# Performance work log

Hardware: AMD Instinct MI355X
Metric: run time of the kernel (lower is better)

Reference implementation:

```python
import jax, jax.numpy as jnp
import numpy as np

B, M, L = 8, 512, 1024          # batch, block_size, attn_lim (max span)
H, K = 512, 8                   # hidden, heads
D = H // K                      # head_dim = 64
RAMP = 32                       # attn_span_len (soft-mask ramp)
SPAN_INIT = 1.0                 # attn_span_init -> full span, skip_len = 0
SCALE = 1.0 / np.sqrt(D)


def _unskew(X):
    # X: [b, M, M+L] -> [b, M, L]  (relative-position unshift via reshape trick)
    b, m, ml = X.shape
    l = ml - m
    X = X.reshape(b, m * ml)
    X = jnp.pad(X, ((0, 0), (0, m)))
    X = X.reshape(b, m, ml + 1)
    return X[:, :, :l]


def _skew(X):
    # X: [b, M, L] -> [b, M, L+M]  (pad value 0)
    b, m, l = X.shape
    X = jnp.pad(X, ((0, 0), (0, 0), (0, m + 1)))
    X = X.reshape(b, -1)[:, : m * (l + m)]
    return X.reshape(b, m, l + m)


def _heads(x):
    # [B, S, H] -> [B*K, S, D]
    b, s, _ = x.shape
    return x.reshape(b, s, K, D).transpose(0, 2, 1, 3).reshape(b * K, s, D)


def setup_inputs() -> dict:
    key0 = jax.random.key(0)
    ks = jax.random.split(key0, 8)
    s = 0.02
    return {
        "query": jax.random.normal(ks[0], (B, M, H), jnp.float32),
        "key": jax.random.normal(ks[1], (B, M + L, H), jnp.float32),
        "value": jax.random.normal(ks[2], (B, M + L, H), jnp.float32),
        "key_pe": jax.random.normal(ks[3], (1, D, L), jnp.float32) * s,
        "Wq": jax.random.normal(ks[4], (H, H), jnp.float32) * s,
        "Wk": jax.random.normal(ks[5], (H, H), jnp.float32) * s,
        "Wv": jax.random.normal(ks[6], (H, H), jnp.float32) * s,
        "Wo": jax.random.normal(ks[7], (H, H), jnp.float32) * s,
        "span_val": jnp.full((K, 1, 1), SPAN_INIT, jnp.float32),
    }


def reference(query, key, value, key_pe, Wq, Wk, Wv, Wo, span_val):
    # QKV projections (nn.Linear, no bias: y = x @ W.T) + head split
    q = _heads(query @ Wq.T)     # [B*K, M, D]
    k = _heads(key @ Wk.T)       # [B*K, M+L, D]
    v = _heads(value @ Wv.T)     # [B*K, M+L, D]

    # content attention + unskew to relative coordinates
    attn_cont = _unskew(jnp.einsum('bmd,bnd->bmn', q, k))    # [B*K, M, L]
    # positional attention (shared across batch/heads via key_pe[1,D,L])
    attn_pos = jnp.einsum('bmd,dl->bml', q, key_pe[0])       # [B*K, M, L]

    attn = jax.nn.softmax((attn_cont + attn_pos) * SCALE, axis=-1)

    # adaptive span soft mask, per head (skip_len = 0)
    template = jnp.linspace(1.0 - L, 0.0, L, dtype=jnp.float32)        # [L]
    mask = jnp.clip((template + span_val * L) / RAMP + 1.0, 0.0, 1.0)  # [K,1,L]
    attn = (attn.reshape(B, K, M, L) * mask[None]).reshape(B * K, M, L)

    # skew back to absolute coords and contract with values
    out = jnp.matmul(_skew(attn), v)                         # [B*K, M, D]
    out = out.reshape(B, K, M, D).transpose(0, 2, 1, 3).reshape(B, M, H)
    return out @ Wo.T
```

## Files before the change

### kernel.cpp

```cpp
#include <hip/hip_runtime.h>
#include <hip/hip_bf16.h>
#include <type_traits>

typedef __hip_bfloat16 bf16;
typedef short bf16x8 __attribute__((ext_vector_type(8)));
typedef float f32x4 __attribute__((ext_vector_type(4)));
typedef short short4_ __attribute__((ext_vector_type(4)));

#define NB 8
#define SM 512
#define SL 1024
#define SH 512
#define NH 8
#define HD 64
#define SN 1536

static __device__ __forceinline__ short bf_bits(float x) {
  union { bf16 b; short s; } u; u.b = __float2bfloat16(x); return u.s;
}
static __device__ __forceinline__ bf16x8 ld8any(const bf16* p) {
  return *reinterpret_cast<const bf16x8*>(p);
}
static __device__ __forceinline__ bf16x8 ld8any(const float* p) {
  float4 a = *reinterpret_cast<const float4*>(p);
  float4 b = *reinterpret_cast<const float4*>(p + 4);
  bf16x8 r;
  r[0] = bf_bits(a.x); r[1] = bf_bits(a.y); r[2] = bf_bits(a.z); r[3] = bf_bits(a.w);
  r[4] = bf_bits(b.x); r[5] = bf_bits(b.y); r[6] = bf_bits(b.z); r[7] = bf_bits(b.w);
  return r;
}
static __device__ __forceinline__ void st1(bf16* p, float v) { *p = __float2bfloat16(v); }
static __device__ __forceinline__ void st1(float* p, float v) { *p = v; }
static __device__ __forceinline__ f32x4 mfma16(bf16x8 a, bf16x8 b, f32x4 c) {
  return __builtin_amdgcn_mfma_f32_16x16x32_bf16(a, b, c, 0, 0, 0);
}


__global__ __launch_bounds__(256) void prep_all(
    const float* __restrict__ key, const float* __restrict__ value,
    const float* __restrict__ query,
    const float* __restrict__ Wq, const float* __restrict__ Wk,
    const float* __restrict__ Wv, const float* __restrict__ Wo,
    const float* __restrict__ pe,
    bf16* __restrict__ kS, bf16* __restrict__ vS, bf16* __restrict__ qS,
    bf16* __restrict__ Wb, bf16* __restrict__ peF) {
  __shared__ __align__(16) bf16 t[16 * 520];
  const int id = blockIdx.x, tid = threadIdx.x;
  if (id < 1920) {
    const float* src; bf16* dst;
    if (id < 768)       { src = key   + (size_t)id * 8192;
                          dst = kS    + (size_t)id * 8192; }
    else if (id < 1536) { src = value + (size_t)(id - 768) * 8192;
                          dst = vS    + (size_t)(id - 768) * 8192; }
    else if (id < 1792) { src = query + (size_t)(id - 1536) * 8192;
                          dst = qS    + (size_t)(id - 1536) * 8192; }
    else {
      const int s = id - 1792;
      const float* ws_[4] = {Wq, Wk, Wv, Wo};
      src = ws_[s >> 5] + (size_t)(s & 31) * 8192;
      dst = Wb + (size_t)(s >> 5) * 262144 + (size_t)(s & 31) * 8192;
    }
#pragma unroll
    for (int j = 0; j < 4; ++j) {
      const int i = j * 2048 + tid * 8;
      const bf16x8 v = ld8any(src + i);
      *reinterpret_cast<bf16x8*>(&t[(i >> 9) * 520 + (i & 511)]) = v;
    }
    __syncthreads();
#pragma unroll
    for (int j = 0; j < 4; ++j) {
      const int a = j * 2048 + tid * 8;
      const int kt5 = a >> 9, rest = a & 511;
      const int q = rest >> 7, rowl = (rest >> 3) & 15;
      *reinterpret_cast<bf16x8*>(dst + a) =
          *reinterpret_cast<const bf16x8*>(&t[rowl * 520 + kt5 * 32 + q * 8]);
    }
  } else {
    const int idx = (id - 1920) * 256 + tid;
    const int l = idx >> 6, d = idx & 63;
    peF[(size_t)((l >> 4) * 2 + (d >> 5)) * 512
        + (size_t)((((d >> 3) & 3) * 16 + (l & 15)) * 8 + (d & 7))]
      = __float2bfloat16(pe[d * SL + l]);
  }
}

#define T2STR 136

#define GL2(AF, BF, KT)                                                      \
  {                                                                          \
    AF[0] = ld8any(xr +         (size_t)(KT) * 512);                         \
    AF[1] = ld8any(xr + 8192  + (size_t)(KT) * 512);                         \
    AF[2] = ld8any(xr + 16384 + (size_t)(KT) * 512);                         \
    AF[3] = ld8any(xr + 24576 + (size_t)(KT) * 512);                         \
    BF[0] = ld8any(wr +         (size_t)(KT) * 512);                         \
    BF[1] = ld8any(wr + 8192  + (size_t)(KT) * 512);                         \
    BF[2] = ld8any(wr + 16384 + (size_t)(KT) * 512);                         \
    BF[3] = ld8any(wr + 24576 + (size_t)(KT) * 512);                         \
  }

#define MF44(AF, BF)                                                         \
  {                                                                          \
    _Pragma("unroll")                                                        \
    for (int mt = 0; mt < 4; ++mt)                                           \
      _Pragma("unroll")                                                      \
      for (int nt = 0; nt < 4; ++nt)                                         \
        acc[mt][nt] = mfma16(AF[mt], BF[nt], acc[mt][nt]);                   \
  }

template <int MODE, typename TY>
static __device__ __forceinline__ void gemm_dev2(const bf16* __restrict__ XF,
                                                 const bf16* __restrict__ WF,
                                                 TY* __restrict__ Y,
                                                 int xblk, int yblk, bf16* tile) {
  const int tid  = threadIdx.x;
  const int lane = tid & 63, w = tid >> 6;
  const int col16 = lane & 15, quad = lane >> 4;
  const int lane8 = lane * 8;
  const int wm = w >> 1, wn = w & 1;
  const int m0 = xblk * 128 + wm * 64;
  const int n0 = yblk * 128 + wn * 64;
  const bf16* xr = XF + (size_t)(m0 >> 4) * 8192 + lane8;
  const bf16* wr = WF + (size_t)(n0 >> 4) * 8192 + lane8;
  f32x4 acc[4][4];
#pragma unroll
  for (int i = 0; i < 4; ++i)
#pragma unroll
    for (int j = 0; j < 4; ++j) acc[i][j] = f32x4{0.f,0.f,0.f,0.f};

  bf16x8 afA[4], bfA[4], afB[4], bfB[4], afC[4], bfC[4];
  GL2(afA, bfA, 0);
  GL2(afB, bfB, 1);
  __builtin_amdgcn_sched_barrier(0);
#pragma unroll
  for (int kt = 0; kt < 16; ++kt) {
    const int nxt = kt + 2;
    if (nxt < 16) {
      if (nxt % 3 == 0)      { GL2(afA, bfA, nxt); }
      else if (nxt % 3 == 1) { GL2(afB, bfB, nxt); }
      else                   { GL2(afC, bfC, nxt); }
      __builtin_amdgcn_sched_barrier(0);
    }
    if (kt % 3 == 0)      MF44(afA, bfA)
    else if (kt % 3 == 1) MF44(afB, bfB)
    else                  MF44(afC, bfC)
  }

  if constexpr (MODE == 0) {
#pragma unroll
    for (int mt = 0; mt < 4; ++mt)
#pragma unroll
      for (int r = 0; r < 4; ++r) {
        const int row = m0 + mt*16 + quad*4 + r;
        TY* yr = Y + (size_t)row * SH + n0 + col16;
#pragma unroll
        for (int nt = 0; nt < 4; ++nt) st1(yr + nt*16, acc[mt][nt][r]);
      }
  } else if constexpr (MODE == 1) {
    const int dq = col16 >> 3, de = col16 & 7;
    const int head = n0 >> 6;
#pragma unroll
    for (int mt = 0; mt < 4; ++mt)
#pragma unroll
      for (int r = 0; r < 4; ++r) {
        const int row = m0 + mt*16 + quad*4 + r;
        const int b = row / SN, sr = row - b * SN;
        bf16* yr = (bf16*)Y
            + (((size_t)(b*NH + head)*96 + (sr>>4))*2)*512
            + (size_t)((sr&15)*8 + de);
#pragma unroll
        for (int nt = 0; nt < 4; ++nt)
          yr[(nt>>1)*512 + ((nt&1)*2 + dq)*128] = __float2bfloat16(acc[mt][nt][r]);
      }
  } else if constexpr (MODE == 3) {
    const int dq = col16 >> 3, de = col16 & 7;
    const int c5b = n0 >> 5;
#pragma unroll
    for (int mt = 0; mt < 4; ++mt)
#pragma unroll
      for (int r = 0; r < 4; ++r) {
        bf16* yr = (bf16*)Y + (size_t)((m0>>4) + mt) * 8192
                 + (size_t)((quad*4 + r)*8 + de);
#pragma unroll
        for (int nt = 0; nt < 4; ++nt)
          yr[(c5b + (nt>>1))*512 + ((nt&1)*2 + dq)*128] = __float2bfloat16(acc[mt][nt][r]);
      }
  } else {
#pragma unroll
    for (int mt = 0; mt < 4; ++mt)
#pragma unroll
      for (int r = 0; r < 4; ++r) {
        const int row_loc = wm*64 + mt*16 + quad*4 + r;
#pragma unroll
        for (int nt = 0; nt < 4; ++nt) {
          const int d = wn*64 + nt*16 + col16;
          tile[d * T2STR + row_loc] = __float2bfloat16(acc[mt][nt][r]);
        }
      }
    __syncthreads();
    const int d  = tid >> 1;
    const int hq = tid & 1;
    const bf16* src = tile + d * T2STR + hq * 64;
    const int row0 = xblk*128 + hq*64;
    const int b = row0 / SN, sr0 = row0 - b * SN;
    const int head = yblk*2 + (d >> 6);
    const int dd = d & 63;
    bf16* dstF = (bf16*)Y + (((size_t)(b*NH + head)*4 + (dd>>4))*96)*256
               + (size_t)(dd&15)*8;
#pragma unroll
    for (int i = 0; i < 8; ++i) {
      const int key = sr0 + i*8;
      const size_t off = (size_t)(key>>4)*256 + (size_t)((key>>3)&1)*128;
      *reinterpret_cast<uint4*>(dstF + off) = reinterpret_cast<const uint4*>(src)[i];
    }
  }
}

static __device__ __forceinline__ void xcd_remap(int lid, int& xblk, int& yblk) {
  xblk = (lid >> 5) * 8 + (lid & 7);
  yblk = (lid >> 3) & 3;
}

__global__ __launch_bounds__(256, 2) void gemmKQ(
    const bf16* __restrict__ XK, const bf16* __restrict__ WK, bf16* __restrict__ YK,
    const bf16* __restrict__ XQ, const bf16* __restrict__ WQ, bf16* __restrict__ YQ) {
  __shared__ bf16 dummy[8];
  const int id = blockIdx.x;
  int xblk, yblk;
  if (id < 384) {
    xcd_remap(id, xblk, yblk);
    gemm_dev2<1, bf16>(XK, WK, YK, xblk, yblk, dummy);
  } else {
    xcd_remap(id - 384, xblk, yblk);
    gemm_dev2<3, bf16>(XQ, WQ, YQ, xblk, yblk, dummy);
  }
}

__global__ __launch_bounds__(256, 2) void gemmV(
    const bf16* __restrict__ XF, const bf16* __restrict__ WF, bf16* __restrict__ Y) {
  __shared__ __align__(16) bf16 tile[128 * T2STR];
  int xblk, yblk;
  xcd_remap(blockIdx.x, xblk, yblk);
  gemm_dev2<2, bf16>(XF, WF, Y, xblk, yblk, tile);
}

#define GLO(AF, BF, KT)                                                      \
  {                                                                          \
    AF[0] = ld8any(xr +         (size_t)(KT) * 512);                         \
    AF[1] = ld8any(xr + 8192  + (size_t)(KT) * 512);                         \
    AF[2] = ld8any(xr + 16384 + (size_t)(KT) * 512);                         \
    AF[3] = ld8any(xr + 24576 + (size_t)(KT) * 512);                         \
    BF[0] = ld8any(wr +         (size_t)(KT) * 512);                         \
    BF[1] = ld8any(wr + 8192  + (size_t)(KT) * 512);                         \
  }

#define MF42(AF, BF)                                                         \
  {                                                                          \
    _Pragma("unroll")                                                        \
    for (int mt = 0; mt < 4; ++mt)                                           \
      _Pragma("unroll")                                                      \
      for (int nt = 0; nt < 2; ++nt)                                         \
        acc[mt][nt] = mfma16(AF[mt], BF[nt], acc[mt][nt]);                   \
  }

__global__ __launch_bounds__(256, 2) void gemmO(
    const bf16* __restrict__ XF, const bf16* __restrict__ WF, float* __restrict__ Y) {
  const int id   = blockIdx.x;
  const int s_   = id >> 3;
  const int xblk = (id & 7) + 8 * (s_ >> 3);
  const int yblk = s_ & 7;
  const int tid  = threadIdx.x;
  const int lane = tid & 63, w = tid >> 6;
  const int col16 = lane & 15, quad = lane >> 4;
  const int lane8 = lane * 8;
  const int wm = w >> 1, wn = w & 1;
  const int m0 = xblk * 128 + wm * 64;
  const int n0 = yblk * 64 + wn * 32;
  const bf16* xr = XF + (size_t)(m0 >> 4) * 8192 + lane8;
  const bf16* wr = WF + (size_t)(n0 >> 4) * 8192 + lane8;
  f32x4 acc[4][2];
#pragma unroll
  for (int i = 0; i < 4; ++i)
#pragma unroll
    for (int j = 0; j < 2; ++j) acc[i][j] = f32x4{0.f,0.f,0.f,0.f};

  bf16x8 afA[4], bfA[2], afB[4], bfB[2], afC[4], bfC[2];
  GLO(afA, bfA, 0);
  GLO(afB, bfB, 1);
  __builtin_amdgcn_sched_barrier(0);
#pragma unroll
  for (int kt = 0; kt < 16; ++kt) {
    const int nxt = kt + 2;
    if (nxt < 16) {
      if (nxt % 3 == 0)      { GLO(afA, bfA, nxt); }
      else if (nxt % 3 == 1) { GLO(afB, bfB, nxt); }
      else                   { GLO(afC, bfC, nxt); }
      __builtin_amdgcn_sched_barrier(0);
    }
    if (kt % 3 == 0)      MF42(afA, bfA)
    else if (kt % 3 == 1) MF42(afB, bfB)
    else                  MF42(afC, bfC)
  }
#pragma unroll
  for (int mt = 0; mt < 4; ++mt)
#pragma unroll
    for (int r = 0; r < 4; ++r) {
      const int row = m0 + mt*16 + quad*4 + r;
      float* yr = Y + (size_t)row * SH + n0 + col16;
      yr[0]  = acc[mt][0][r];
      yr[16] = acc[mt][1][r];
    }
}

#define PSTR1 69
#define BSTR1 104

__global__ __launch_bounds__(64, 2) void attn1w(
    const bf16* __restrict__ qp, const bf16* __restrict__ Kh,
    const bf16* __restrict__ VT, const bf16* __restrict__ peT,
    const float* __restrict__ spanv, bf16* __restrict__ ctx) {
  __shared__ __align__(16) float pos_s[16 * PSTR1];
  __shared__ __align__(16) bf16  P_s[16 * BSTR1];

  const int id = blockIdx.x;
  const int h  = id & 7;
  const int s_ = id >> 3;
  const int m0 = (s_ & 31) * 16;
  const int b  = s_ >> 5;
  const int hb = b * 8 + h;
  const int lane  = threadIdx.x;
  const int col16 = lane & 15, quad = lane >> 4, kq = quad << 3;
  const int q4 = quad << 2;
  const int lane8 = lane * 8;

  for (int i = lane; i < 16 * BSTR1; i += 64)
    P_s[i] = __float2bfloat16(0.0f);

  const bf16* qb = qp + (size_t)((b*SM + m0) >> 4) * 8192 + h*1024 + lane8;
  const bf16x8 qf0 = ld8any(qb), qf1 = ld8any(qb + 512);

  const bf16* kbF = Kh + (size_t)hb * 98304 + lane8;
  const bf16* vbF = VT + (size_t)hb * 98304 + lane8;
  const bf16* pbF = peT + lane8;

  float Mrun = -1.0e30f, Srun = 0.0f;
  const float span1024 = spanv[h] * 1024.0f;
  f32x4 o[4];
#pragma unroll
  for (int dt = 0; dt < 4; ++dt) o[dt] = f32x4{0.f,0.f,0.f,0.f};

  float bias_[5][4], mvs_[5][4];
  {
    const float mvb = ((float)(q4 - col16 - 1023) + span1024) * 0.03125f + 1.0f;
#pragma unroll
    for (int t = 0; t < 5; ++t)
#pragma unroll
      for (int r = 0; r < 4; ++r) {
        const int l = 16*t + q4 + r - col16;
        bias_[t][r] = ((unsigned)l < 64u) ? 0.0f : -1.0e30f;
        mvs_[t][r]  = mvb + (float)(16*t + r) * 0.03125f;
      }
  }

  bf16x8 kf[5][2], pf[4][2], vf[4][3];

  {
    const int tk0 = m0 >> 4;
#pragma unroll
    for (int t = 0; t < 5; ++t) {
      const bf16* kr = kbF + (size_t)(tk0 + t) * 1024;
      kf[t][0] = ld8any(kr); kf[t][1] = ld8any(kr + 512);
    }
#pragma unroll
    for (int t = 0; t < 4; ++t) {
      const bf16* pr = pbF + (size_t)t * 1024;
      pf[t][0] = ld8any(pr); pf[t][1] = ld8any(pr + 512);
    }
#pragma unroll
    for (int dt = 0; dt < 4; ++dt) {
      const bf16* v0 = vbF + (size_t)dt * 24576 + (size_t)tk0 * 256;
#pragma unroll
      for (int ks = 0; ks < 3; ++ks) vf[dt][ks] = ld8any(v0 + ks*512);
    }
    __builtin_amdgcn_sched_barrier(0);
  }

  const int posw = col16 * PSTR1 + q4;
  const int posr = col16 * (PSTR1 - 1) + q4;
  const int pww  = col16 * BSTR1 + q4;
  const int pwr  = col16 * BSTR1 + kq;

  for (int ch = 0; ch < 16; ++ch) {
    const int l0 = ch << 6;

    f32x4 pacc[4];
#pragma unroll
    for (int t = 0; t < 4; ++t) {
      f32x4 a = {0.f,0.f,0.f,0.f};
      a = mfma16(pf[t][0], qf0, a);
      a = mfma16(pf[t][1], qf1, a);
      pacc[t] = a;
    }
#pragma unroll
    for (int t = 0; t < 4; ++t)
#pragma unroll
      for (int r = 0; r < 4; ++r)
        pos_s[posw + 16*t + r] = pacc[t][r];

    f32x4 cacc[5];
#pragma unroll
    for (int t = 0; t < 5; ++t) {
      f32x4 a = {0.f,0.f,0.f,0.f};
      a = mfma16(kf[t][0], qf0, a);
      a = mfma16(kf[t][1], qf1, a);
      cacc[t] = a;
    }

    {
      const int l0n = (ch < 15) ? l0 + 64 : l0;
      const int tkn = (m0 + l0n) >> 4;
      const int tpn = l0n >> 4;
#pragma unroll
      for (int t = 0; t < 5; ++t) {
        const bf16* kr = kbF + (size_t)(tkn + t) * 1024;
        kf[t][0] = ld8any(kr); kf[t][1] = ld8any(kr + 512);
      }
#pragma unroll
      for (int t = 0; t < 4; ++t) {
        const bf16* pr = pbF + (size_t)(tpn + t) * 1024;
        pf[t][0] = ld8any(pr); pf[t][1] = ld8any(pr + 512);
      }
      __builtin_amdgcn_sched_barrier(0);
    }

    float sc[5][4];
    float mc = -1.0e30f;
#pragma unroll
    for (int t = 0; t < 5; ++t) {
      const f32x4 pv4 = *reinterpret_cast<const f32x4*>(&pos_s[posr + 16*t]);
#pragma unroll
      for (int r = 0; r < 4; ++r) {
        const float v = fmaf(cacc[t][r] + pv4[r], 0.125f, bias_[t][r]);
        sc[t][r] = v;
        mc = fmaxf(mc, v);
      }
    }
    mc = fmaxf(mc, __shfl_xor(mc, 16));
    mc = fmaxf(mc, __shfl_xor(mc, 32));
    const float Mnew = fmaxf(Mrun, mc);
    const bool defer = __all(Mnew - Mrun <= 8.0f);
    const float Mb = defer ? Mrun : Mnew;
    const float chf = (float)ch * 2.0f;
    float ls = 0.0f;
#pragma unroll
    for (int t = 0; t < 5; ++t) {
      short4_ pk;
#pragma unroll
      for (int r = 0; r < 4; ++r) {
        const float p = __expf(sc[t][r] - Mb);
        ls += p;
        float mv = mvs_[t][r] + chf;
        mv = fminf(fmaxf(mv, 0.0f), 1.0f);
        pk[r] = bf_bits(p * mv);
      }
      *reinterpret_cast<short4_*>(&P_s[pww + 16*t]) = pk;
    }
    ls += __shfl_xor(ls, 16);
    ls += __shfl_xor(ls, 32);

    if (defer) {
      Srun += ls;
    } else {
      const float alpha = __expf(Mrun - Mnew);
      Srun = Srun * alpha + ls;
      Mrun = Mnew;
#pragma unroll
      for (int dt = 0; dt < 4; ++dt)
#pragma unroll
        for (int r = 0; r < 4; ++r) o[dt][r] *= alpha;
    }

#pragma unroll
    for (int ks = 0; ks < 3; ++ks) {
      const bf16x8 ap = ld8any(&P_s[pwr + ks*32]);
#pragma unroll
      for (int dt = 0; dt < 4; ++dt)
        o[dt] = mfma16(vf[dt][ks], ap, o[dt]);
    }

    {
      const int tkn = (m0 + ((ch < 15) ? l0 + 64 : l0)) >> 4;
#pragma unroll
      for (int dt = 0; dt < 4; ++dt) {
        const bf16* v0 = vbF + (size_t)dt * 24576 + (size_t)tkn * 256;
#pragma unroll
        for (int ks = 0; ks < 3; ++ks) vf[dt][ks] = ld8any(v0 + ks*512);
      }
      __builtin_amdgcn_sched_barrier(0);
    }
  }

  const float inv = 1.0f / Srun;
  bf16* crb = ctx + (size_t)((b*SM + m0) >> 4) * 8192
            + (size_t)(h*1024 + (quad>>1)*128 + col16*8 + (quad&1)*4);
#pragma unroll
  for (int dt = 0; dt < 4; ++dt) {
    short4_ pk;
#pragma unroll
    for (int r = 0; r < 4; ++r) pk[r] = bf_bits(o[dt][r] * inv);
    *reinterpret_cast<short4_*>(crb + (size_t)(dt>>1)*512 + (dt&1)*256) = pk;
  }
}

template <int MODE, typename TX, typename TW, typename TY>
__global__ __launch_bounds__(256) void gemmbn64(const TX* __restrict__ X,
                                                const TW* __restrict__ W,
                                                TY* __restrict__ Y) {
  __shared__ __align__(16) bf16 tile[(MODE == 2) ? 64 * T2STR : 8];
  const int id   = blockIdx.x;
  const int s_   = id >> 3;
  const int xblk = (id & 7) + 8 * (s_ >> 3);
  const int yblk = s_ & 7;
  const int tid  = threadIdx.x;
  const int lane = tid & 63, w = tid >> 6;
  const int col16 = lane & 15, quad = lane >> 4, kq = quad << 3;
  const int wm = w >> 1, wn = w & 1;
  const int m0 = xblk * 128 + wm * 64;
  const int n0 = yblk * 64 + wn * 32;
  const TX* xr = X + (size_t)(m0 + col16) * SH + kq;
  const TW* wr = W + (size_t)(n0 + col16) * SH + kq;
  f32x4 acc[4][2];
#pragma unroll
  for (int i = 0; i < 4; ++i)
#pragma unroll
    for (int j = 0; j < 2; ++j) acc[i][j] = f32x4{0.f,0.f,0.f,0.f};
#pragma unroll
  for (int k0 = 0; k0 < SH; k0 += 32) {
    bf16x8 af[4], bfr[2];
#pragma unroll
    for (int t = 0; t < 4; ++t) af[t]  = ld8any(xr + (size_t)(t*16) * SH + k0);
#pragma unroll
    for (int t = 0; t < 2; ++t) bfr[t] = ld8any(wr + (size_t)(t*16) * SH + k0);
#pragma unroll
    for (int mt = 0; mt < 4; ++mt)
#pragma unroll
      for (int nt = 0; nt < 2; ++nt)
        acc[mt][nt] = mfma16(af[mt], bfr[nt], acc[mt][nt]);
  }

  if constexpr (MODE == 0) {
#pragma unroll
    for (int mt = 0; mt < 4; ++mt)
#pragma unroll
      for (int r = 0; r < 4; ++r) {
        const int row = m0 + mt*16 + quad*4 + r;
        TY* yr = Y + (size_t)row * SH + n0 + col16;
        st1(yr,      acc[mt][0][r]);
        st1(yr + 16, acc[mt][1][r]);
      }
  } else if constexpr (MODE == 1) {
#pragma unroll
    for (int mt = 0; mt < 4; ++mt)
#pragma unroll
      for (int r = 0; r < 4; ++r) {
        const int row = m0 + mt*16 + quad*4 + r;
        const int b = row / SN, sr = row - b * SN;
        bf16* yr = (bf16*)Y + (size_t)((b*NH + yblk)*SN + sr) * HD
                 + wn*32 + col16;
        yr[0]  = __float2bfloat16(acc[mt][0][r]);
        yr[16] = __float2bfloat16(acc[mt][1][r]);
      }
  } else {
#pragma unroll
    for (int mt = 0; mt < 4; ++mt)
#pragma unroll
      for (int r = 0; r < 4; ++r) {
        const int row_loc = wm*64 + mt*16 + quad*4 + r;
#pragma unroll
        for (int nt = 0; nt < 2; ++nt) {
          const int d = wn*32 + nt*16 + col16;
          tile[d * T2STR + row_loc] = __float2bfloat16(acc[mt][nt][r]);
        }
      }
    __syncthreads();
    const int d  = tid >> 2;
    const int hq = tid & 3;
    const bf16* src = tile + d * T2STR + hq * 32;
    const int row0 = xblk*128 + hq*32;
    const int b = row0 / SN, sr0 = row0 - b * SN;
    bf16* dst = (bf16*)Y + (size_t)((b*NH + yblk)*HD + d) * SN + sr0;
#pragma unroll
    for (int i = 0; i < 4; ++i)
      reinterpret_cast<uint4*>(dst)[i] = reinterpret_cast<const uint4*>(src)[i];
  }
}

__global__ void transpose_pe_fb(const float* __restrict__ pe, bf16* __restrict__ peT) {
  int idx = blockIdx.x * 256 + threadIdx.x;
  int l = idx >> 6, d = idx & 63;
  peT[idx] = __float2bfloat16(pe[d * SL + l]);
}

#define MT 16
#define CSTR 84
#define PSTR 65
#define BSTR 104
#define QSTR 72

__global__ __launch_bounds__(128) void attn_kernel_fb(
    const float* __restrict__ query, const float* __restrict__ Wq,
    const bf16* __restrict__ Kh, const bf16* __restrict__ VT,
    const bf16* __restrict__ peT, const float* __restrict__ spanv,
    bf16* __restrict__ ctx) {
  __shared__ __align__(16) float cont_lds[MT][CSTR];
  __shared__ __align__(16) float pos_lds[MT][PSTR];
  __shared__ __align__(16) bf16  P_lds[MT][BSTR];
  __shared__ __align__(16) bf16  q_lds[MT*QSTR];
  __shared__ float alpha_lds[MT];
  __shared__ float S_lds[MT];

  const int id = blockIdx.x;
  const int h  = id & 7;
  const int s_ = id >> 3;
  const int m0 = (s_ & 31) * MT;
  const int b  = s_ >> 5;
  const int hb = b * 8 + h;
  const int tid  = threadIdx.x;
  const int lane = tid & 63;
  const int w    = tid >> 6;
  const int col16 = lane & 15, quad = lane >> 4, kq = quad << 3;
  const int wr = quad << 2;

  for (int i = tid; i < MT * BSTR; i += 128)
    (&P_lds[0][0])[i] = __float2bfloat16(0.0f);

  bf16x8 qf0, qf1;
  {
    f32x4 qa0 = {0.f,0.f,0.f,0.f}, qa1 = qa0;
    const float* xq = query + (size_t)(b*SM + m0 + col16) * SH + kq;
    const float* w0 = Wq + (size_t)(h*HD + w*32 + col16) * SH + kq;
    const float* w1 = w0 + (size_t)16 * SH;
#pragma unroll
    for (int k0 = 0; k0 < SH; k0 += 32) {
      bf16x8 xa = ld8any(xq + k0);
      qa0 = mfma16(xa, ld8any(w0 + k0), qa0);
      qa1 = mfma16(xa, ld8any(w1 + k0), qa1);
    }
#pragma unroll
    for (int r = 0; r < 4; ++r) {
      q_lds[(wr + r)*QSTR + w*32 + col16]      = __float2bfloat16(qa0[r]);
      q_lds[(wr + r)*QSTR + w*32 + 16 + col16] = __float2bfloat16(qa1[r]);
    }
    __syncthreads();
    qf0 = ld8any(&q_lds[col16*QSTR + kq]);
    qf1 = ld8any(&q_lds[col16*QSTR + kq + 32]);
  }

  const bf16* kb = Kh + (size_t)(hb * SN) * HD + kq;
  const bf16* vb = VT + (size_t)(hb * HD) * SN;

  const int srow = tid >> 3, sj = tid & 7;
  float Mrun = -1.0e30f, Srun = 0.0f;
  const float span = spanv[h];
  const int dt0 = w * 16, dt1 = (w + 2) * 16;
  f32x4 o0 = {0.f,0.f,0.f,0.f}, o1 = o0;

  for (int ch = 0; ch < 16; ++ch) {
    const int l0 = ch << 6;
    const int nb_ = m0 + l0;

    f32x4 ca0 = {0.f,0.f,0.f,0.f}, ca1 = ca0, ca2 = ca0, pa0 = ca0, pa1 = ca0;
    {
      const bf16* kr0 = kb + (size_t)(nb_ + w*16 + col16) * HD;
      ca0 = mfma16(qf0, ld8any(kr0),           ca0);
      ca0 = mfma16(qf1, ld8any(kr0 + 32),      ca0);
      const bf16* kr1 = kr0 + 32 * HD;
      ca1 = mfma16(qf0, ld8any(kr1),           ca1);
      ca1 = mfma16(qf1, ld8any(kr1 + 32),      ca1);
      if (w == 0) {
        const bf16* kr2 = kr0 + 64 * HD;
        ca2 = mfma16(qf0, ld8any(kr2),         ca2);
        ca2 = mfma16(qf1, ld8any(kr2 + 32),    ca2);
      }
      const bf16* pr0 = peT + (size_t)(l0 + w*16 + col16) * HD + kq;
      pa0 = mfma16(qf0, ld8any(pr0),           pa0);
      pa0 = mfma16(qf1, ld8any(pr0 + 32),      pa0);
      const bf16* pr1 = pr0 + 32 * HD;
      pa1 = mfma16(qf0, ld8any(pr1),           pa1);
      pa1 = mfma16(qf1, ld8any(pr1 + 32),      pa1);
    }
#pragma unroll
    for (int r = 0; r < 4; ++r) {
      cont_lds[wr + r][w*16 + col16]      = ca0[r];
      cont_lds[wr + r][w*16 + 32 + col16] = ca1[r];
      if (w == 0) cont_lds[wr + r][64 + col16] = ca2[r];
      pos_lds[wr + r][w*16 + col16]       = pa0[r];
      pos_lds[wr + r][w*16 + 32 + col16]  = pa1[r];
    }
    __syncthreads();

    float sc[8];
    float mc = -1.0e30f;
    const float* crow = &cont_lds[srow][srow + sj*8];
    const float* prow = &pos_lds[srow][sj*8];
#pragma unroll
    for (int i = 0; i < 8; ++i) {
      float v = (crow[i] + prow[i]) * 0.125f;
      sc[i] = v;
      mc = fmaxf(mc, v);
    }
    mc = fmaxf(mc, __shfl_xor(mc, 1));
    mc = fmaxf(mc, __shfl_xor(mc, 2));
    mc = fmaxf(mc, __shfl_xor(mc, 4));
    const float Mnew = fmaxf(Mrun, mc);
    const float alpha = __expf(Mrun - Mnew);
    float ls = 0.0f;
    bf16* pwrow = &P_lds[srow][srow + sj*8];
#pragma unroll
    for (int i = 0; i < 8; ++i) {
      float p = __expf(sc[i] - Mnew);
      ls += p;
      const float tpl = (float)(l0 + sj*8 + i) - 1023.0f;
      float mv = (tpl + span * 1024.0f) * 0.03125f + 1.0f;
      mv = fminf(fmaxf(mv, 0.0f), 1.0f);
      pwrow[i] = __float2bfloat16(p * mv);
    }
    ls += __shfl_xor(ls, 1);
    ls += __shfl_xor(ls, 2);
    ls += __shfl_xor(ls, 4);
    Srun = Srun * alpha + ls;
    Mrun = Mnew;
    if (sj == 0) { alpha_lds[srow] = alpha; S_lds[srow] = Srun; }
    __syncthreads();

    float al[4];
#pragma unroll
    for (int r = 0; r < 4; ++r) al[r] = alpha_lds[wr + r];
#pragma unroll
    for (int r = 0; r < 4; ++r) { o0[r] *= al[r]; o1[r] *= al[r]; }
#pragma unroll
    for (int ks = 0; ks < 3; ++ks) {
      const bf16x8 ap = ld8any(&P_lds[col16][ks*32 + kq]);
      const bf16* v0 = vb + (size_t)(dt0 + col16) * SN + nb_ + ks*32 + kq;
      const bf16* v1 = vb + (size_t)(dt1 + col16) * SN + nb_ + ks*32 + kq;
      o0 = mfma16(ap, ld8any(v0), o0);
      o1 = mfma16(ap, ld8any(v1), o1);
    }
  }

  bf16* cr = ctx + (size_t)(b*SM + m0 + wr) * SH + h*HD + col16;
#pragma unroll
  for (int r = 0; r < 4; ++r) {
    const float inv = 1.0f / S_lds[wr + r];
    cr[(size_t)r * SH + dt0] = __float2bfloat16(o0[r] * inv);
    cr[(size_t)r * SH + dt1] = __float2bfloat16(o1[r] * inv);
  }
}

extern "C" void kernel_launch(void* const* d_in, const int* in_sizes, int n_in,
                              void* d_out, int out_size, void* d_ws, size_t ws_size,
                              hipStream_t stream) {
  const float* query  = (const float*)d_in[0];
  const float* key    = (const float*)d_in[1];
  const float* value  = (const float*)d_in[2];
  const float* key_pe = (const float*)d_in[3];
  const float* Wq     = (const float*)d_in[4];
  const float* Wk     = (const float*)d_in[5];
  const float* Wv     = (const float*)d_in[6];
  const float* Wo     = (const float*)d_in[7];
  const float* spanv  = (const float*)d_in[8];
  float* out = (float*)d_out;

  bf16* ws = (bf16*)d_ws;
  if (ws_size >= (size_t)48365568) {
    bf16* B0   = ws;
    bf16* B1   = B0  + 6291456;
    bf16* B2   = B1  + 6291456;
    bf16* qp   = B2  + 6291456;
    bf16* ctxC = qp  + 2097152;
    bf16* peF  = ctxC + 2097152;
    bf16* Wb   = peF + 65536;
    bf16* Wq_b = Wb, *Wk_b = Wb + 262144, *Wv_b = Wb + 524288, *Wo_b = Wb + 786432;

    prep_all<<<2176, 256, 0, stream>>>(key, value, query, Wq, Wk, Wv, Wo,
                                       key_pe, B0, B1, ctxC, Wb, peF);
    gemmKQ<<<512, 256, 0, stream>>>(B0, Wk_b, B2, ctxC, Wq_b, qp);
    gemmV<<<384, 256, 0, stream>>>(B1, Wv_b, B0);
    attn1w<<<2048, 64, 0, stream>>>(qp, B2, B0, peF, spanv, ctxC);
    gemmO<<<256, 256, 0, stream>>>(ctxC, Wo_b, out);
  } else {
    bf16* k_head = ws;
    bf16* vT     = k_head + 6291456;
    bf16* ctx    = vT     + 6291456;
    bf16* peT    = ctx    + 2097152;
    gemmbn64<1, float, float, bf16><<<768, 256, 0, stream>>>(key,   Wk, k_head);
    gemmbn64<2, float, float, bf16><<<768, 256, 0, stream>>>(value, Wv, vT);
    transpose_pe_fb<<<256, 256, 0, stream>>>(key_pe, peT);
    attn_kernel_fb<<<2048, 128, 0, stream>>>(query, Wq, k_head, vT,
                                             peT, spanv, ctx);
    gemmbn64<0, bf16, float, float><<<256, 256, 0, stream>>>(ctx, Wo, out);
  }
}
```

Baseline: 182.8 us.

## Merge K/Q/V projection GEMMs into one launch and reuse overlapping attention tiles

Combines the K/Q projection kernel and the V projection kernel into a single 896-block launch. V now writes to a new workspace buffer so it no longer has to wait for B0 to be consumed. In the attention loop, the K and V fragments that overlap between consecutive 64-wide chunks are carried forward in registers instead of being reloaded. This cuts one kernel launch and some global loads, at the cost of a larger workspace requirement and slightly more register shuffling.

New measurement: 172.4 us. 5.7% less time.

```diff
diff --git a/kernel.cpp b/kernel.cpp
--- a/kernel.cpp
+++ b/kernel.cpp
@@ -243,6 +243,25 @@
   gemm_dev2<2, bf16>(XF, WF, Y, xblk, yblk, tile);
 }
 
+__global__ __launch_bounds__(256, 2) void gemmKQV3(
+    const bf16* __restrict__ XK, const bf16* __restrict__ WK, bf16* __restrict__ YK,
+    const bf16* __restrict__ XQ, const bf16* __restrict__ WQ, bf16* __restrict__ YQ,
+    const bf16* __restrict__ XV, const bf16* __restrict__ WV, bf16* __restrict__ YV) {
+  __shared__ __align__(16) bf16 tile[128 * T2STR];
+  const int id = blockIdx.x;
+  int xblk, yblk;
+  if (id < 384) {
+    xcd_remap(id, xblk, yblk);
+    gemm_dev2<1, bf16>(XK, WK, YK, xblk, yblk, tile);
+  } else if (id < 512) {
+    xcd_remap(id - 384, xblk, yblk);
+    gemm_dev2<3, bf16>(XQ, WQ, YQ, xblk, yblk, tile);
+  } else {
+    xcd_remap(id - 512, xblk, yblk);
+    gemm_dev2<2, bf16>(XV, WV, YV, xblk, yblk, tile);
+  }
+}
+
 #define GLO(AF, BF, KT)                                                      \
   {                                                                          \
     AF[0] = ld8any(xr +         (size_t)(KT) * 512);                         \
@@ -419,11 +438,13 @@
       const int l0n = (ch < 15) ? l0 + 64 : l0;
       const int tkn = (m0 + l0n) >> 4;
       const int tpn = l0n >> 4;
-#pragma unroll
-      for (int t = 0; t < 5; ++t) {
+      const bf16x8 kc0 = kf[4][0], kc1 = kf[4][1];
+#pragma unroll
+      for (int t = 1; t < 5; ++t) {
         const bf16* kr = kbF + (size_t)(tkn + t) * 1024;
         kf[t][0] = ld8any(kr); kf[t][1] = ld8any(kr + 512);
       }
+      kf[0][0] = kc0; kf[0][1] = kc1;
 #pragma unroll
       for (int t = 0; t < 4; ++t) {
         const bf16* pr = pbF + (size_t)(tpn + t) * 1024;
@@ -491,9 +512,11 @@
       const int tkn = (m0 + ((ch < 15) ? l0 + 64 : l0)) >> 4;
 #pragma unroll
       for (int dt = 0; dt < 4; ++dt) {
+        const bf16x8 vc = vf[dt][2];
         const bf16* v0 = vbF + (size_t)dt * 24576 + (size_t)tkn * 256;
-#pragma unroll
-        for (int ks = 0; ks < 3; ++ks) vf[dt][ks] = ld8any(v0 + ks*512);
+        vf[dt][1] = ld8any(v0 + 512);
+        vf[dt][2] = ld8any(v0 + 1024);
+        vf[dt][0] = vc;
       }
       __builtin_amdgcn_sched_barrier(0);
     }
@@ -771,7 +794,24 @@
   float* out = (float*)d_out;
 
   bf16* ws = (bf16*)d_ws;
-  if (ws_size >= (size_t)48365568) {
+  if (ws_size >= (size_t)60948480) {
+    bf16* B0   = ws;
+    bf16* B1   = B0  + 6291456;
+    bf16* B2   = B1  + 6291456;
+    bf16* B3   = B2  + 6291456;
+    bf16* qp   = B3  + 6291456;
+    bf16* ctxC = qp  + 2097152;
+    bf16* peF  = ctxC + 2097152;
+    bf16* Wb   = peF + 65536;
+    bf16* Wq_b = Wb, *Wk_b = Wb + 262144, *Wv_b = Wb + 524288, *Wo_b = Wb + 786432;
+
+    prep_all<<<2176, 256, 0, stream>>>(key, value, query, Wq, Wk, Wv, Wo,
+                                       key_pe, B0, B1, ctxC, Wb, peF);
+    gemmKQV3<<<896, 256, 0, stream>>>(B0, Wk_b, B2, ctxC, Wq_b, qp,
+                                      B1, Wv_b, B3);
+    attn1w<<<2048, 64, 0, stream>>>(qp, B2, B3, peF, spanv, ctxC);
+    gemmO<<<256, 256, 0, stream>>>(ctxC, Wo_b, out);
+  } else if (ws_size >= (size_t)48365568) {
     bf16* B0   = ws;
     bf16* B1   = B0  + 6291456;
     bf16* B2   = B1  + 6291456;
```
